# Kernel tuning notes

Measured on AMD Instinct MI355X. Metric: run time of the kernel, lower is better.

Reference implementation:

```python
import jax, jax.numpy as jnp
from jax import lax
import numpy as np

T, B, D, H = 2048, 64, 512, 512  # time, batch, input_size, hidden_size


def setup_inputs() -> dict:
    key = jax.random.key(0)
    k1, k2, k3, k4, k5 = jax.random.split(key, 5)
    s = 1.0 / np.sqrt(H)
    inputs = jax.random.normal(k1, (T, B, D), dtype=jnp.float32)
    W_ih = jax.random.uniform(k2, (4 * H, D), minval=-s, maxval=s, dtype=jnp.float32)
    W_hh = jax.random.uniform(k3, (4 * H, H), minval=-s, maxval=s, dtype=jnp.float32)
    b_ih = jax.random.uniform(k4, (4 * H,), minval=-s, maxval=s, dtype=jnp.float32)
    b_hh = jax.random.uniform(k5, (4 * H,), minval=-s, maxval=s, dtype=jnp.float32)
    return {"inputs": inputs, "W_ih": W_ih, "W_hh": W_hh, "b_ih": b_ih, "b_hh": b_hh}


def reference(inputs, W_ih, W_hh, b_ih, b_hh):
    # TimeRecurrentCell with batch_first=False, lstm=True, no attention, no reverse:
    # hidden=None -> zero-initialized (h, c); loop over time feeding an LSTM cell,
    # stacking per-step outputs along the time dim. Expressed as lax.scan.
    hidden = W_hh.shape[1]
    batch = inputs.shape[1]
    h0 = jnp.zeros((batch, hidden), dtype=inputs.dtype)
    c0 = jnp.zeros((batch, hidden), dtype=inputs.dtype)

    def step(carry, x_t):  # x_t: [B, D]
        h, c = carry
        gates = x_t @ W_ih.T + b_ih + h @ W_hh.T + b_hh  # [B, 4H]
        i, f, g, o = jnp.split(gates, 4, axis=-1)  # torch LSTMCell gate order
        i = jax.nn.sigmoid(i)
        f = jax.nn.sigmoid(f)
        g = jnp.tanh(g)
        o = jax.nn.sigmoid(o)
        c_new = f * c + i * g
        h_new = o * jnp.tanh(c_new)
        return (h_new, c_new), h_new

    (h_T, c_T), outputs = lax.scan(step, (h0, c0), inputs)  # outputs: [T, B, H]
    return outputs, (h_T, c_T)
```

## Files before the change

### kernel.cpp

```cpp
#include <hip/hip_runtime.h>
#include <hip/hip_bf16.h>
#include <hip/hip_fp16.h>

#define TT 2048
#define BB 64
#define HH 512
#define GG 2048

typedef __attribute__((ext_vector_type(4))) float f32x4;
typedef __attribute__((ext_vector_type(8))) short short8;
typedef __attribute__((ext_vector_type(4))) short short4v;
typedef __attribute__((ext_vector_type(4))) unsigned u32x4;
typedef unsigned long long ull;

static __device__ __forceinline__ short f2bf(float f) {
  unsigned u = __builtin_bit_cast(unsigned, f);
  u = (u + 0x7FFFu + ((u >> 16) & 1u)) >> 16;
  return (short)u;
}
static __device__ __forceinline__ float fsigmoid(float x) { return 1.0f / (1.0f + __expf(-x)); }
static __device__ __forceinline__ float ftanh(float x) {
  float e = __expf(2.0f * x);
  return 1.0f - 2.0f / (e + 1.0f);
}
static __device__ __forceinline__ float h2f(unsigned short u) {
  __half h = __builtin_bit_cast(__half, u);
  return __half2float(h);
}

__global__ void cvt_bf16_kernel(const float4* __restrict__ in, short4v* __restrict__ outp, long n4) {
  long i = (long)blockIdx.x * blockDim.x + threadIdx.x;
  long stride = (long)gridDim.x * blockDim.x;
  for (; i < n4; i += stride) {
    float4 v = in[i];
    short4v o;
    o[0] = f2bf(v.x); o[1] = f2bf(v.y); o[2] = f2bf(v.z); o[3] = f2bf(v.w);
    outp[i] = o;
  }
}

__global__ void init_flags(unsigned* flags) {
  __hip_atomic_store(flags + threadIdx.x, 0u, __ATOMIC_RELAXED, __HIP_MEMORY_SCOPE_AGENT);
}

__global__ __launch_bounds__(256) void gemm_xpart(
    const __hip_bfloat16* __restrict__ Abf, const __hip_bfloat16* __restrict__ Bbf,
    const float* __restrict__ bih, const float* __restrict__ bhh, __half* __restrict__ xout) {
  __shared__ __hip_bfloat16 As[128 * 64];
  __shared__ __hip_bfloat16 Bs[128 * 64];
  const int nwg = gridDim.x;
  const int bid = blockIdx.x;
  const int vb = (bid & 7) * (nwg >> 3) + (bid >> 3);
  const int mt = vb >> 4;
  const int nt = vb & 15;
  const size_t m0 = (size_t)mt * 128;
  const int n0 = nt * 128;
  const int tid = threadIdx.x;
  const int lane = tid & 63;
  const int w = tid >> 6;
  const int wm = w >> 1, wn = w & 1;
  const int g = lane >> 4;
  const int l15 = lane & 15;
  f32x4 acc[4][4] = {};
  for (int k0 = 0; k0 < 512; k0 += 64) {
#pragma unroll
    for (int i = 0; i < 4; i++) {
      const int slot = w * 4 + i;
      const int row = slot * 8 + (lane >> 3);
      const int segS = (lane & 7) ^ (row & 7);
      const __hip_bfloat16* ga = Abf + (m0 + row) * 512 + k0 + segS * 8;
      const __hip_bfloat16* gb = Bbf + (size_t)(n0 + row) * 512 + k0 + segS * 8;
      __builtin_amdgcn_global_load_lds(
          (const __attribute__((address_space(1))) unsigned*)(const void*)ga,
          (__attribute__((address_space(3))) unsigned*)(void*)(As + slot * 512), 16, 0, 0);
      __builtin_amdgcn_global_load_lds(
          (const __attribute__((address_space(1))) unsigned*)(const void*)gb,
          (__attribute__((address_space(3))) unsigned*)(void*)(Bs + slot * 512), 16, 0, 0);
    }
    __syncthreads();
#pragma unroll
    for (int kk = 0; kk < 2; kk++) {
      short8 av[4], bv[4];
#pragma unroll
      for (int f = 0; f < 4; f++) {
        const int row = wm * 64 + f * 16 + l15;
        av[f] = *(const short8*)(As + row * 64 + ((((kk << 2) + g) ^ (row & 7)) << 3));
      }
#pragma unroll
      for (int f = 0; f < 4; f++) {
        const int row = wn * 64 + f * 16 + l15;
        bv[f] = *(const short8*)(Bs + row * 64 + ((((kk << 2) + g) ^ (row & 7)) << 3));
      }
#pragma unroll
      for (int fi = 0; fi < 4; fi++)
#pragma unroll
        for (int fj = 0; fj < 4; fj++)
          acc[fi][fj] = __builtin_amdgcn_mfma_f32_16x16x32_bf16(av[fi], bv[fj], acc[fi][fj], 0, 0, 0);
    }
    __syncthreads();
  }
  const int q = nt >> 2;
  const int gt = mt * 2 + wm;
#pragma unroll
  for (int fj = 0; fj < 4; fj++) {
    const int n = n0 + wn * 64 + fj * 16 + l15;
    const float bias = bih[n] + bhh[n];
    const int cp = (nt & 3) * 2 + wn;
    const int slot = fj >> 1;
    const int wpart = (fj & 1) * 4 + (l15 >> 2);
    const int g4s = l15 & 3;
#pragma unroll
    for (int fi = 0; fi < 4; fi++) {
#pragma unroll
      for (int r = 0; r < 4; r++) {
        const int b16 = g * 4 + r;
        const int thr = wpart * 64 + g4s * 16 + b16;
        const size_t hidx = ((((size_t)gt * 4 + q) * 4 + fi) * 8 + cp) * 1024 + thr * 2 + slot;
        xout[hidx] = __float2half(acc[fi][fj][r] + bias);
      }
    }
  }
}

__global__ __launch_bounds__(512, 2) void lstm_scan_kernel(
    const __half* __restrict__ xpart, const float* __restrict__ Whh,
    char* hbuf, float* __restrict__ outp, unsigned* flags) {
  __shared__ char Hs[16384];
  const int blk = blockIdx.x;
  const int bg = blk >> 3;
  const int cp = blk & 7;
  const int tid = threadIdx.x;
  const int lane = tid & 63;
  const int w = tid >> 6;
  const int b16 = lane & 15;
  const int g4 = lane >> 4;
  const int qr = b16 & 3;
  const int jj = b16 >> 2;
  const int colA = cp * 64 + w * 4 + g4;
  const int colB = cp * 64 + (w + 8) * 4 + g4;
  const int batchg = bg * 16 + b16;

  const int rowA = qr * 512 + cp * 64 + w * 4 + jj;
  const int rowB = qr * 512 + cp * 64 + (w + 8) * 4 + jj;
  short8 wA[16], wB[16];
#pragma unroll
  for (int kt = 0; kt < 16; kt++) {
    const float* pa = Whh + (size_t)rowA * 512 + kt * 32 + g4 * 8;
    const float* pb = Whh + (size_t)rowB * 512 + kt * 32 + g4 * 8;
    float4 a0 = *(const float4*)pa;
    float4 a1 = *(const float4*)(pa + 4);
    float4 b0 = *(const float4*)pb;
    float4 b1 = *(const float4*)(pb + 4);
    short8 va, vb;
    va[0] = f2bf(a0.x); va[1] = f2bf(a0.y); va[2] = f2bf(a0.z); va[3] = f2bf(a0.w);
    va[4] = f2bf(a1.x); va[5] = f2bf(a1.y); va[6] = f2bf(a1.z); va[7] = f2bf(a1.w);
    vb[0] = f2bf(b0.x); vb[1] = f2bf(b0.y); vb[2] = f2bf(b0.z); vb[3] = f2bf(b0.w);
    vb[4] = f2bf(b1.x); vb[5] = f2bf(b1.y); vb[6] = f2bf(b1.z); vb[7] = f2bf(b1.w);
    wA[kt] = va;
    wB[kt] = vb;
  }

  const ull xroot = (ull)(uintptr_t)xpart + ((ull)(bg * 8 + cp) * 512 + (ull)tid) * 4ull;
  const ull qstep = 4ull * 8 * 512 * 4;
  const ull xstep = 4ull * qstep;
  const ull hroot = (ull)(uintptr_t)hbuf + (ull)(bg * 16384);
  unsigned* fbase = flags + bg * 8;

  unsigned xq0, xq1, xq2, xq3, xn0, xn1, xn2, xn3;
  asm volatile("global_load_dword %0, %1, off" : "=v"(xq0) : "v"(xroot));
  asm volatile("global_load_dword %0, %1, off" : "=v"(xq1) : "v"(xroot + qstep));
  asm volatile("global_load_dword %0, %1, off" : "=v"(xq2) : "v"(xroot + 2 * qstep));
  asm volatile("global_load_dword %0, %1, off" : "=v"(xq3) : "v"(xroot + 3 * qstep));
  asm volatile("s_waitcnt vmcnt(0)" ::: "memory");

  float cA = 0.f, cB = 0.f, hAv = 0.f, hBv = 0.f;

  for (int t = 0; t < TT; t++) {
    f32x4 accA = {0.f, 0.f, 0.f, 0.f};
    f32x4 accB = {0.f, 0.f, 0.f, 0.f};
    if (t > 0) {
      if (w == 0) {
        unsigned f;
        do {
          f = __hip_atomic_load(fbase + (lane & 7), __ATOMIC_RELAXED, __HIP_MEMORY_SCOPE_AGENT);
        } while (!__all((int)(f >= (unsigned)t)));
      }
      __syncthreads();
      const ull hb = hroot + (ull)((t & 1) * 65536);
      u32x4 hv[2];
#pragma unroll
      for (int p = 0; p < 2; p++) {
        const ull a = hb + (ull)((p * 8 + w) * 1024 + lane * 16);
        asm volatile("global_load_dwordx4 %0, %1, off sc0 sc1" : "=v"(hv[p]) : "v"(a));
      }
      asm volatile("s_waitcnt vmcnt(0)" ::: "memory");
      __builtin_amdgcn_sched_barrier(0);
#pragma unroll
      for (int p = 0; p < 2; p++) {
        const int b = p * 8 + w;
        *(u32x4*)(Hs + b * 1024 + ((lane ^ (b & 7)) << 4)) = hv[p];
      }
      __syncthreads();
#pragma unroll
      for (int kt = 0; kt < 16; kt++) {
        const int sp = ((kt * 4 + g4) ^ (b16 & 7));
        short8 hf = *(const short8*)(Hs + b16 * 1024 + (sp << 4));
        accA = __builtin_amdgcn_mfma_f32_16x16x32_bf16(wA[kt], hf, accA, 0, 0, 0);
        accB = __builtin_amdgcn_mfma_f32_16x16x32_bf16(wB[kt], hf, accB, 0, 0, 0);
      }
    }

    float iA = fsigmoid(accA[0] + h2f((unsigned short)(xq0 & 0xFFFF)));
    float fA = fsigmoid(accA[1] + h2f((unsigned short)(xq1 & 0xFFFF)));
    float gA = ftanh(accA[2] + h2f((unsigned short)(xq2 & 0xFFFF)));
    float oA = fsigmoid(accA[3] + h2f((unsigned short)(xq3 & 0xFFFF)));
    cA = fA * cA + iA * gA;
    hAv = oA * ftanh(cA);
    float iB = fsigmoid(accB[0] + h2f((unsigned short)(xq0 >> 16)));
    float fB = fsigmoid(accB[1] + h2f((unsigned short)(xq1 >> 16)));
    float gB = ftanh(accB[2] + h2f((unsigned short)(xq2 >> 16)));
    float oB = fsigmoid(accB[3] + h2f((unsigned short)(xq3 >> 16)));
    cB = fB * cB + iB * gB;
    hBv = oB * ftanh(cB);

    float hAp = __shfl_xor(hAv, 16, 64);
    float hBp = __shfl_xor(hBv, 16, 64);
    if ((g4 & 1) == 0) {
      unsigned* hd = (unsigned*)(hbuf + ((t + 1) & 1) * 65536 + bg * 16384 + b16 * 1024);
      unsigned pkA = (unsigned)(unsigned short)f2bf(hAv) | ((unsigned)(unsigned short)f2bf(hAp) << 16);
      unsigned pkB = (unsigned)(unsigned short)f2bf(hBv) | ((unsigned)(unsigned short)f2bf(hBp) << 16);
      __hip_atomic_store(hd + (colA >> 1), pkA, __ATOMIC_RELAXED, __HIP_MEMORY_SCOPE_AGENT);
      __hip_atomic_store(hd + (colB >> 1), pkB, __ATOMIC_RELAXED, __HIP_MEMORY_SCOPE_AGENT);
    }
    asm volatile("s_waitcnt vmcnt(0)" ::: "memory");
    __syncthreads();
    if (tid == 0)
      __hip_atomic_store(fbase + cp, (unsigned)(t + 1), __ATOMIC_RELAXED, __HIP_MEMORY_SCOPE_AGENT);

    const ull pfb = xroot + (ull)(t + 1 < TT ? t + 1 : TT - 1) * xstep;
    asm volatile("global_load_dword %0, %1, off" : "=v"(xn0) : "v"(pfb));
    asm volatile("global_load_dword %0, %1, off" : "=v"(xn1) : "v"(pfb + qstep));
    asm volatile("global_load_dword %0, %1, off" : "=v"(xn2) : "v"(pfb + 2 * qstep));
    asm volatile("global_load_dword %0, %1, off" : "=v"(xn3) : "v"(pfb + 3 * qstep));

    float* od = outp + ((size_t)t * BB + batchg) * HH;
    od[colA] = hAv;
    od[colB] = hBv;
    xq0 = xn0; xq1 = xn1; xq2 = xn2; xq3 = xn3;
  }

  float* hT = outp + (size_t)TT * BB * HH;
  float* cT = hT + (size_t)BB * HH;
  hT[(size_t)batchg * HH + colA] = hAv;
  hT[(size_t)batchg * HH + colB] = hBv;
  cT[(size_t)batchg * HH + colA] = cA;
  cT[(size_t)batchg * HH + colB] = cB;
}

extern "C" void kernel_launch(void* const* d_in, const int* in_sizes, int n_in,
                              void* d_out, int out_size, void* d_ws, size_t ws_size,
                              hipStream_t stream) {
  (void)in_sizes; (void)n_in; (void)out_size; (void)ws_size;
  const float* x = (const float*)d_in[0];
  const float* Wih = (const float*)d_in[1];
  const float* Whh = (const float*)d_in[2];
  const float* bih = (const float*)d_in[3];
  const float* bhh = (const float*)d_in[4];
  float* outp = (float*)d_out;
  char* ws = (char*)d_ws;

  const size_t M = (size_t)TT * BB;
  size_t off = 0;
  auto take = [&](size_t sz) { size_t r = off; off = (off + sz + 255) & ~255ULL; return r; };
  const size_t xbf_o = take(M * 512 * 2);
  const size_t wih_o = take((size_t)GG * 512 * 2);
  const size_t hbuf_o = take(2 * 65536);
  const size_t flg_o = take(256);
  const size_t xpart_o = take(M * (size_t)GG * 2);

  __hip_bfloat16* xbf = (__hip_bfloat16*)(ws + xbf_o);
  __hip_bfloat16* wihbf = (__hip_bfloat16*)(ws + wih_o);
  __half* xpart = (__half*)(ws + xpart_o);

  hipMemsetAsync(ws + hbuf_o, 0, 2 * 65536, stream);
  init_flags<<<1, 64, 0, stream>>>((unsigned*)(ws + flg_o));
  cvt_bf16_kernel<<<4096, 256, 0, stream>>>((const float4*)x, (short4v*)xbf, (long)(M * 512 / 4));
  cvt_bf16_kernel<<<256, 256, 0, stream>>>((const float4*)Wih, (short4v*)wihbf, (long)((size_t)GG * 512 / 4));

  gemm_xpart<<<16384, 256, 0, stream>>>(xbf, wihbf, bih, bhh, xpart);
  lstm_scan_kernel<<<32, 512, 0, stream>>>(xpart, Whh, ws + hbuf_o, outp, (unsigned*)(ws + flg_o));
}
```

Baseline: 7.857 ms.

## Fuse input-projection GEMM and LSTM scan into one persistent kernel with readiness counters

Merges the x@W_ih GEMM and the recurrent scan into a single launch. The first 32 blocks run the scan and the rest compute GEMM tiles, with per-M-tile ready counters letting the scan start as soon as its timesteps' projections are written, so the GEMM overlaps the serial recurrence. GEMM stores are also packed into dword writes. The cost is 512-thread blocks for GEMM work where half the threads sit idle, plus polling overhead inside the scan loop. Progress depends on the scan blocks being resident alongside the GEMM blocks.

Measured after the change: 7.521 ms, median of 2. 4.3% less time.

```diff
diff --git a/kernel.cpp b/kernel.cpp
--- a/kernel.cpp
+++ b/kernel.cpp
@@ -39,18 +39,20 @@
   }
 }
 
-__global__ void init_flags(unsigned* flags) {
-  __hip_atomic_store(flags + threadIdx.x, 0u, __ATOMIC_RELAXED, __HIP_MEMORY_SCOPE_AGENT);
-}
-
-__global__ __launch_bounds__(256) void gemm_xpart(
+__global__ void init_sync(unsigned* base) {
+  int i = blockIdx.x * 256 + threadIdx.x;
+  if (i < 1088)
+    __hip_atomic_store(base + i, 0u, __ATOMIC_RELAXED, __HIP_MEMORY_SCOPE_AGENT);
+}
+
+
+__device__ __forceinline__ void gemm_part(
+    char* smem, int vb,
     const __hip_bfloat16* __restrict__ Abf, const __hip_bfloat16* __restrict__ Bbf,
-    const float* __restrict__ bih, const float* __restrict__ bhh, __half* __restrict__ xout) {
-  __shared__ __hip_bfloat16 As[128 * 64];
-  __shared__ __hip_bfloat16 Bs[128 * 64];
-  const int nwg = gridDim.x;
-  const int bid = blockIdx.x;
-  const int vb = (bid & 7) * (nwg >> 3) + (bid >> 3);
+    const float* __restrict__ bih, const float* __restrict__ bhh,
+    char* xpart, unsigned* ready) {
+  __hip_bfloat16* As = (__hip_bfloat16*)smem;
+  __hip_bfloat16* Bs = As + 8192;
   const int mt = vb >> 4;
   const int nt = vb & 15;
   const size_t m0 = (size_t)mt * 128;
@@ -63,69 +65,84 @@
   const int l15 = lane & 15;
   f32x4 acc[4][4] = {};
   for (int k0 = 0; k0 < 512; k0 += 64) {
-#pragma unroll
-    for (int i = 0; i < 4; i++) {
-      const int slot = w * 4 + i;
-      const int row = slot * 8 + (lane >> 3);
-      const int segS = (lane & 7) ^ (row & 7);
-      const __hip_bfloat16* ga = Abf + (m0 + row) * 512 + k0 + segS * 8;
-      const __hip_bfloat16* gb = Bbf + (size_t)(n0 + row) * 512 + k0 + segS * 8;
-      __builtin_amdgcn_global_load_lds(
-          (const __attribute__((address_space(1))) unsigned*)(const void*)ga,
-          (__attribute__((address_space(3))) unsigned*)(void*)(As + slot * 512), 16, 0, 0);
-      __builtin_amdgcn_global_load_lds(
-          (const __attribute__((address_space(1))) unsigned*)(const void*)gb,
-          (__attribute__((address_space(3))) unsigned*)(void*)(Bs + slot * 512), 16, 0, 0);
+    if (tid < 256) {
+#pragma unroll
+      for (int i = 0; i < 4; i++) {
+        const int slot = w * 4 + i;
+        const int row = slot * 8 + (lane >> 3);
+        const int segS = (lane & 7) ^ (row & 7);
+        const __hip_bfloat16* ga = Abf + (m0 + row) * 512 + k0 + segS * 8;
+        const __hip_bfloat16* gb = Bbf + (size_t)(n0 + row) * 512 + k0 + segS * 8;
+        __builtin_amdgcn_global_load_lds(
+            (const __attribute__((address_space(1))) unsigned*)(const void*)ga,
+            (__attribute__((address_space(3))) unsigned*)(void*)(As + slot * 512), 16, 0, 0);
+        __builtin_amdgcn_global_load_lds(
+            (const __attribute__((address_space(1))) unsigned*)(const void*)gb,
+            (__attribute__((address_space(3))) unsigned*)(void*)(Bs + slot * 512), 16, 0, 0);
+      }
     }
     __syncthreads();
-#pragma unroll
-    for (int kk = 0; kk < 2; kk++) {
-      short8 av[4], bv[4];
-#pragma unroll
-      for (int f = 0; f < 4; f++) {
-        const int row = wm * 64 + f * 16 + l15;
-        av[f] = *(const short8*)(As + row * 64 + ((((kk << 2) + g) ^ (row & 7)) << 3));
-      }
-#pragma unroll
-      for (int f = 0; f < 4; f++) {
-        const int row = wn * 64 + f * 16 + l15;
-        bv[f] = *(const short8*)(Bs + row * 64 + ((((kk << 2) + g) ^ (row & 7)) << 3));
-      }
-#pragma unroll
-      for (int fi = 0; fi < 4; fi++)
-#pragma unroll
-        for (int fj = 0; fj < 4; fj++)
-          acc[fi][fj] = __builtin_amdgcn_mfma_f32_16x16x32_bf16(av[fi], bv[fj], acc[fi][fj], 0, 0, 0);
+    if (tid < 256) {
+#pragma unroll
+      for (int kk = 0; kk < 2; kk++) {
+        short8 av[4], bv[4];
+#pragma unroll
+        for (int f = 0; f < 4; f++) {
+          const int row = wm * 64 + f * 16 + l15;
+          av[f] = *(const short8*)(As + row * 64 + ((((kk << 2) + g) ^ (row & 7)) << 3));
+        }
+#pragma unroll
+        for (int f = 0; f < 4; f++) {
+          const int row = wn * 64 + f * 16 + l15;
+          bv[f] = *(const short8*)(Bs + row * 64 + ((((kk << 2) + g) ^ (row & 7)) << 3));
+        }
+#pragma unroll
+        for (int fi = 0; fi < 4; fi++)
+#pragma unroll
+          for (int fj = 0; fj < 4; fj++)
+            acc[fi][fj] = __builtin_amdgcn_mfma_f32_16x16x32_bf16(av[fi], bv[fj], acc[fi][fj], 0, 0, 0);
+      }
     }
     __syncthreads();
   }
-  const int q = nt >> 2;
-  const int gt = mt * 2 + wm;
-#pragma unroll
-  for (int fj = 0; fj < 4; fj++) {
-    const int n = n0 + wn * 64 + fj * 16 + l15;
-    const float bias = bih[n] + bhh[n];
+  if (tid < 256) {
+    const int q = nt >> 2;
+    const int gt = mt * 2 + wm;
     const int cp = (nt & 3) * 2 + wn;
-    const int slot = fj >> 1;
-    const int wpart = (fj & 1) * 4 + (l15 >> 2);
     const int g4s = l15 & 3;
 #pragma unroll
-    for (int fi = 0; fi < 4; fi++) {
-#pragma unroll
-      for (int r = 0; r < 4; r++) {
-        const int b16 = g * 4 + r;
-        const int thr = wpart * 64 + g4s * 16 + b16;
-        const size_t hidx = ((((size_t)gt * 4 + q) * 4 + fi) * 8 + cp) * 1024 + thr * 2 + slot;
-        xout[hidx] = __float2half(acc[fi][fj][r] + bias);
-      }
-    }
-  }
-}
-
-__global__ __launch_bounds__(512, 2) void lstm_scan_kernel(
-    const __half* __restrict__ xpart, const float* __restrict__ Whh,
-    char* hbuf, float* __restrict__ outp, unsigned* flags) {
-  __shared__ char Hs[16384];
+    for (int fjp = 0; fjp < 2; fjp++) {
+      const int nlo = n0 + wn * 64 + fjp * 16 + l15;
+      const int nhi = nlo + 32;
+      const float bLo = bih[nlo] + bhh[nlo];
+      const float bHi = bih[nhi] + bhh[nhi];
+      const int wpart = fjp * 4 + (l15 >> 2);
+#pragma unroll
+      for (int fi = 0; fi < 4; fi++) {
+#pragma unroll
+        for (int r = 0; r < 4; r++) {
+          const int thr = wpart * 64 + g4s * 16 + (g * 4 + r);
+          __half lo = __float2half(acc[fi][fjp][r] + bLo);
+          __half hi = __float2half(acc[fi][fjp + 2][r] + bHi);
+          unsigned d = (unsigned)__builtin_bit_cast(unsigned short, lo) |
+                       ((unsigned)__builtin_bit_cast(unsigned short, hi) << 16);
+          const ull dwi = ((((ull)gt * 4 + q) * 4 + fi) * 8 + cp) * 512 + (ull)thr;
+          const ull ga = (ull)(uintptr_t)xpart + dwi * 4ull;
+          asm volatile("global_store_dword %0, %1, off sc0 sc1" ::"v"(ga), "v"(d));
+        }
+      }
+    }
+    asm volatile("s_waitcnt vmcnt(0)" ::: "memory");
+  }
+  __syncthreads();
+  if (tid == 0)
+    __hip_atomic_fetch_add(ready + mt, 1u, __ATOMIC_RELAXED, __HIP_MEMORY_SCOPE_AGENT);
+}
+
+__device__ __forceinline__ void scan_part(
+    char* smem, const char* xpart, const float* __restrict__ Whh,
+    char* hbuf, float* __restrict__ outp, unsigned* flags, unsigned* ready) {
+  char* Hs = smem;
   const int blk = blockIdx.x;
   const int bg = blk >> 3;
   const int cp = blk & 7;
@@ -164,8 +181,16 @@
   const ull qstep = 4ull * 8 * 512 * 4;
   const ull xstep = 4ull * qstep;
   const ull hroot = (ull)(uintptr_t)hbuf + (ull)(bg * 16384);
+  const ull rdroot = (ull)(uintptr_t)ready;
   unsigned* fbase = flags + bg * 8;
 
+  {
+    unsigned rv;
+    do {
+      asm volatile("global_load_dword %0, %1, off sc0 sc1" : "=v"(rv) : "v"(rdroot));
+      asm volatile("s_waitcnt vmcnt(0)" ::: "memory");
+    } while (!__all((int)(rv >= 16u)));
+  }
   unsigned xq0, xq1, xq2, xq3, xn0, xn1, xn2, xn3;
   asm volatile("global_load_dword %0, %1, off" : "=v"(xq0) : "v"(xroot));
   asm volatile("global_load_dword %0, %1, off" : "=v"(xq1) : "v"(xroot + qstep));
@@ -173,6 +198,7 @@
   asm volatile("global_load_dword %0, %1, off" : "=v"(xq3) : "v"(xroot + 3 * qstep));
   asm volatile("s_waitcnt vmcnt(0)" ::: "memory");
 
+  int tile_ok = 0;
   float cA = 0.f, cB = 0.f, hAv = 0.f, hBv = 0.f;
 
   for (int t = 0; t < TT; t++) {
@@ -237,7 +263,26 @@
     if (tid == 0)
       __hip_atomic_store(fbase + cp, (unsigned)(t + 1), __ATOMIC_RELAXED, __HIP_MEMORY_SCOPE_AGENT);
 
-    const ull pfb = xroot + (ull)(t + 1 < TT ? t + 1 : TT - 1) * xstep;
+    const int tn = (t + 1 < TT) ? (t + 1) : (TT - 1);
+    const int tneed = tn >> 1;
+    int ttarget = tneed + 4;
+    if (ttarget > 1023) ttarget = 1023;
+    while (tile_ok < tneed) {
+      unsigned rv;
+      asm volatile("global_load_dword %0, %1, off sc0 sc1"
+                   : "=v"(rv) : "v"(rdroot + (ull)(tile_ok + 1) * 4ull));
+      asm volatile("s_waitcnt vmcnt(0)" ::: "memory");
+      if (__all((int)(rv >= 16u))) tile_ok++;
+    }
+    if (tile_ok < ttarget) {
+      unsigned rv;
+      asm volatile("global_load_dword %0, %1, off sc0 sc1"
+                   : "=v"(rv) : "v"(rdroot + (ull)(tile_ok + 1) * 4ull));
+      asm volatile("s_waitcnt vmcnt(0)" ::: "memory");
+      if (__all((int)(rv >= 16u))) tile_ok++;
+    }
+
+    const ull pfb = xroot + (ull)tn * xstep;
     asm volatile("global_load_dword %0, %1, off" : "=v"(xn0) : "v"(pfb));
     asm volatile("global_load_dword %0, %1, off" : "=v"(xn1) : "v"(pfb + qstep));
     asm volatile("global_load_dword %0, %1, off" : "=v"(xn2) : "v"(pfb + 2 * qstep));
@@ -255,6 +300,20 @@
   hT[(size_t)batchg * HH + colB] = hBv;
   cT[(size_t)batchg * HH + colA] = cA;
   cT[(size_t)batchg * HH + colB] = cB;
+}
+
+__global__ __launch_bounds__(512, 2) void mega_kernel(
+    const __hip_bfloat16* __restrict__ Abf, const __hip_bfloat16* __restrict__ Bbf,
+    const float* __restrict__ bih, const float* __restrict__ bhh,
+    const float* __restrict__ Whh, char* xpart, char* hbuf,
+    float* __restrict__ outp, unsigned* sync) {
+  __shared__ char smem[32768];
+  unsigned* flags = sync;
+  unsigned* ready = sync + 64;
+  if (blockIdx.x < 32)
+    scan_part(smem, xpart, Whh, hbuf, outp, flags, ready);
+  else
+    gemm_part(smem, blockIdx.x - 32, Abf, Bbf, bih, bhh, xpart, ready);
 }
 
 extern "C" void kernel_launch(void* const* d_in, const int* in_sizes, int n_in,
@@ -275,18 +334,18 @@
   const size_t xbf_o = take(M * 512 * 2);
   const size_t wih_o = take((size_t)GG * 512 * 2);
   const size_t hbuf_o = take(2 * 65536);
-  const size_t flg_o = take(256);
+  const size_t syn_o = take(4608);
   const size_t xpart_o = take(M * (size_t)GG * 2);
 
   __hip_bfloat16* xbf = (__hip_bfloat16*)(ws + xbf_o);
   __hip_bfloat16* wihbf = (__hip_bfloat16*)(ws + wih_o);
-  __half* xpart = (__half*)(ws + xpart_o);
 
   hipMemsetAsync(ws + hbuf_o, 0, 2 * 65536, stream);
-  init_flags<<<1, 64, 0, stream>>>((unsigned*)(ws + flg_o));
+  init_sync<<<5, 256, 0, stream>>>((unsigned*)(ws + syn_o));
   cvt_bf16_kernel<<<4096, 256, 0, stream>>>((const float4*)x, (short4v*)xbf, (long)(M * 512 / 4));
   cvt_bf16_kernel<<<256, 256, 0, stream>>>((const float4*)Wih, (short4v*)wihbf, (long)((size_t)GG * 512 / 4));
 
-  gemm_xpart<<<16384, 256, 0, stream>>>(xbf, wihbf, bih, bhh, xpart);
-  lstm_scan_kernel<<<32, 512, 0, stream>>>(xpart, Whh, ws + hbuf_o, outp, (unsigned*)(ws + flg_o));
-}
+  mega_kernel<<<32 + 16384, 512, 0, stream>>>(xbf, wihbf, bih, bhh, Whh,
+                                              ws + xpart_o, ws + hbuf_o, outp,
+                                              (unsigned*)(ws + syn_o));
+}
```
